# Optimization experiments

Hardware: AMD Instinct MI355X
Metric: run time of the kernel (lower is better)

The kernel has to match this reference:

```python
import jax, jax.numpy as jnp
import numpy as np

N = 100000   # nodes
E = 800000   # edges
D = 64       # feature dim (input=hidden=output)
EPS = 1e-5   # BatchNorm eps


def setup_inputs() -> dict:
    key = jax.random.key(0)
    ks = jax.random.split(key, 24)
    s = 1.0 / np.sqrt(D)
    inp = {
        "x": jax.random.normal(ks[0], (N, D), jnp.float32),
        "edge_index": jax.random.randint(ks[1], (2, E), 0, N, jnp.int64),
        # GCNConv weights (x @ W + b after normalized aggregation)
        "W1": jax.random.normal(ks[2], (D, D), jnp.float32) * s,
        "b1": jax.random.normal(ks[3], (D,), jnp.float32) * 0.01,
        "W2": jax.random.normal(ks[4], (D, D), jnp.float32) * s,
        "b2": jax.random.normal(ks[5], (D,), jnp.float32) * 0.01,
        "W3": jax.random.normal(ks[6], (D, D), jnp.float32) * s,
        "b3": jax.random.normal(ks[7], (D,), jnp.float32) * 0.01,
        # BatchNorm1d (inference: running stats)
        "bn1_g": jax.random.uniform(ks[8], (D,), jnp.float32, 0.5, 1.5),
        "bn1_b": jax.random.normal(ks[9], (D,), jnp.float32) * 0.1,
        "bn1_m": jax.random.normal(ks[10], (D,), jnp.float32) * 0.1,
        "bn1_v": jax.random.uniform(ks[11], (D,), jnp.float32, 0.5, 1.5),
        "bn2_g": jax.random.uniform(ks[12], (D,), jnp.float32, 0.5, 1.5),
        "bn2_b": jax.random.normal(ks[13], (D,), jnp.float32) * 0.1,
        "bn2_m": jax.random.normal(ks[14], (D,), jnp.float32) * 0.1,
        "bn2_v": jax.random.uniform(ks[15], (D,), jnp.float32, 0.5, 1.5),
        # predictor MLP: Linear -> tanh -> (dropout=id) -> Linear
        "pW1": jax.random.normal(ks[16], (D, D), jnp.float32) * s,
        "pb1": jax.random.normal(ks[17], (D,), jnp.float32) * 0.01,
        "pW2": jax.random.normal(ks[18], (D, D), jnp.float32) * s,
        "pb2": jax.random.normal(ks[19], (D,), jnp.float32) * 0.01,
    }
    return inp


def _gcn_norm(edge_index):
    # add self loops, compute sym-normalized edge coefficients (PyG GCNConv)
    loop = jnp.arange(N, dtype=edge_index.dtype)
    src = jnp.concatenate([edge_index[0], loop])
    dst = jnp.concatenate([edge_index[1], loop])
    deg = jax.ops.segment_sum(jnp.ones(src.shape[0], jnp.float32), dst, num_segments=N)
    dis = jax.lax.rsqrt(deg)  # deg >= 1 due to self loops
    norm = dis[src] * dis[dst]
    return src, dst, norm


def _gcn_layer(x, src, dst, norm, W, b):
    h = x @ W                              # [N, D] small GEMM
    msg = h[src] * norm[:, None]           # [E+N, D] gather (memory bound)
    return jax.ops.segment_sum(msg, dst, num_segments=N) + b  # scatter-add


def _bn(x, g, b, m, v):
    return (x - m) * (g * jax.lax.rsqrt(v + EPS)) + b


def reference(x, edge_index, W1, b1, W2, b2, W3, b3,
              bn1_g, bn1_b, bn1_m, bn1_v, bn2_g, bn2_b, bn2_m, bn2_v,
              pW1, pb1, pW2, pb2):
    src, dst, norm = _gcn_norm(edge_index)
    h = _gcn_layer(x, src, dst, norm, W1, b1)
    h = jax.nn.relu(_bn(h, bn1_g, bn1_b, bn1_m, bn1_v))   # dropout = id (eval)
    h = _gcn_layer(h, src, dst, norm, W2, b2)
    h = jax.nn.relu(_bn(h, bn2_g, bn2_b, bn2_m, bn2_v))
    h = _gcn_layer(h, src, dst, norm, W3, b3)
    out = jnp.tanh(h @ pW1 + pb1) @ pW2 + pb2              # predictor MLP
    return out
```

## Files before the change

### kernel.cpp

```cpp
#include <hip/hip_runtime.h>
#include <hip/hip_fp16.h>

#define N_NODES 100000
#define N_EDGES 800000
#define DIM 64
#define BN_EPS 1e-5f
#define LDX 68
#define EDGE_CAP 1600000

__global__ __launch_bounds__(256) void k_cvt_count(const float* __restrict__ x,
                                                   __half* __restrict__ xh,
                                                   const int* __restrict__ dst,
                                                   int* __restrict__ deg) {
    int idx = blockIdx.x * blockDim.x + threadIdx.x;
    if (idx < 1600000) {
        float4 v = ((const float4*)x)[idx];
        unsigned int u0 = __half_as_ushort(__float2half(v.x));
        unsigned int u1 = __half_as_ushort(__float2half(v.y));
        unsigned int u2 = __half_as_ushort(__float2half(v.z));
        unsigned int u3 = __half_as_ushort(__float2half(v.w));
        ((uint2*)xh)[idx] = make_uint2(u0 | (u1 << 16), u2 | (u3 << 16));
    }
    if (idx < N_EDGES) atomicAdd(&deg[dst[idx]], 1);
}

__global__ __launch_bounds__(256) void k_scan_fuse(const int* __restrict__ deg,
                                                   int* __restrict__ row_off,
                                                   int* __restrict__ cursor,
                                                   float* __restrict__ dinv,
                                                   int* __restrict__ gcount,
                                                   const float* __restrict__ W3,
                                                   const float* __restrict__ b3,
                                                   const float* __restrict__ pW1,
                                                   const float* __restrict__ pb1,
                                                   float* __restrict__ W3p,
                                                   float* __restrict__ b3p) {
    int tid = threadIdx.x;
    if (blockIdx.x == 98) {
        int c = tid & 63;
        int kbase = (tid >> 6) * 16;
        for (int k = kbase; k < kbase + 16; ++k) {
            float acc = 0.f;
#pragma unroll 8
            for (int j = 0; j < 64; ++j)
                acc = fmaf(W3[k * 64 + j], pW1[j * 64 + c], acc);
            W3p[k * 64 + c] = acc;
        }
        if (tid < 64) {
            float acc = pb1[c];
#pragma unroll 8
            for (int j = 0; j < 64; ++j)
                acc = fmaf(b3[j], pW1[j * 64 + c], acc);
            b3p[c] = acc;
        }
        return;
    }
    __shared__ int sdata[256];
    __shared__ int sbase;
    int base = blockIdx.x * 1024 + tid * 4;
    int4 d = make_int4(0, 0, 0, 0);
    int4 v = make_int4(0, 0, 0, 0);
    if (base < N_NODES) {
        d = *(const int4*)(deg + base);
        v.x = (d.x + 7) & ~7;
        v.y = (d.y + 7) & ~7;
        v.z = (d.z + 7) & ~7;
        v.w = (d.w + 7) & ~7;
    }
    int tsum = v.x + v.y + v.z + v.w;
    sdata[tid] = tsum;
    __syncthreads();
    for (int off = 1; off < 256; off <<= 1) {
        int t = (tid >= off) ? sdata[tid - off] : 0;
        __syncthreads();
        sdata[tid] += t;
        __syncthreads();
    }
    if (tid == 255) sbase = atomicAdd(gcount, sdata[255]);
    __syncthreads();
    if (base >= N_NODES) return;
    int excl = sdata[tid] - tsum + sbase;
    int4 o;
    o.x = excl;
    o.y = o.x + v.x;
    o.z = o.y + v.y;
    o.w = o.z + v.z;
    *(int4*)(row_off + base) = o;
    *(int4*)(cursor + base) = o;
    float4 di;
    di.x = rsqrtf((float)(d.x + 1));
    di.y = rsqrtf((float)(d.y + 1));
    di.z = rsqrtf((float)(d.z + 1));
    di.w = rsqrtf((float)(d.w + 1));
    *(float4*)(dinv + base) = di;
}

__global__ __launch_bounds__(256) void k_build(const int* __restrict__ ei,
                                               const float* __restrict__ dinv,
                                               int* __restrict__ cursor,
                                               int2* __restrict__ edges) {
    int part = blockIdx.x & 7;
    int e = (blockIdx.x >> 3) * 256 + threadIdx.x;
    if (e >= N_EDGES) return;
    int d = ei[N_EDGES + e];
    if (d / 12500 != part) return;
    int s = ei[e];
    int pos = atomicAdd(&cursor[d], 1);
    edges[pos] = make_int2(s, __float_as_int(dinv[s] * dinv[d]));
}

__global__ __launch_bounds__(256) void k_aggregate(const __half* __restrict__ xin,
                                                   const int* __restrict__ row_off,
                                                   const int* __restrict__ deg,
                                                   const int2* __restrict__ edges,
                                                   const float* __restrict__ dinv,
                                                   __half* __restrict__ out) {
    int lane = threadIdx.x & 63;
    int node = blockIdx.x * 4 + (threadIdx.x >> 6);
    float di = dinv[node];
    float acc = __half2float(xin[(size_t)node * DIM + lane]) * (di * di);
    int beg = __builtin_amdgcn_readfirstlane(row_off[node]);
    int lenp = (__builtin_amdgcn_readfirstlane(deg[node]) + 7) & ~7;
    int end = beg + lenp;
    for (int k = beg; k < end; k += 8) {
        int2 e0 = edges[k + 0];
        int2 e1 = edges[k + 1];
        int2 e2 = edges[k + 2];
        int2 e3 = edges[k + 3];
        int2 e4 = edges[k + 4];
        int2 e5 = edges[k + 5];
        int2 e6 = edges[k + 6];
        int2 e7 = edges[k + 7];
        float v0 = __half2float(xin[(size_t)e0.x * DIM + lane]);
        float v1 = __half2float(xin[(size_t)e1.x * DIM + lane]);
        float v2 = __half2float(xin[(size_t)e2.x * DIM + lane]);
        float v3 = __half2float(xin[(size_t)e3.x * DIM + lane]);
        float v4 = __half2float(xin[(size_t)e4.x * DIM + lane]);
        float v5 = __half2float(xin[(size_t)e5.x * DIM + lane]);
        float v6 = __half2float(xin[(size_t)e6.x * DIM + lane]);
        float v7 = __half2float(xin[(size_t)e7.x * DIM + lane]);
        acc = fmaf(__int_as_float(e0.y), v0, acc);
        acc = fmaf(__int_as_float(e1.y), v1, acc);
        acc = fmaf(__int_as_float(e2.y), v2, acc);
        acc = fmaf(__int_as_float(e3.y), v3, acc);
        acc = fmaf(__int_as_float(e4.y), v4, acc);
        acc = fmaf(__int_as_float(e5.y), v5, acc);
        acc = fmaf(__int_as_float(e6.y), v6, acc);
        acc = fmaf(__int_as_float(e7.y), v7, acc);
    }
    out[(size_t)node * DIM + lane] = __float2half(acc);
}

#define GEMM_STEP(SX, SW)                                                      \
    {                                                                          \
        float4 a0 = *(const float4*)&SX[(r0 + 0) * LDX + k4 * 4];              \
        float4 a1 = *(const float4*)&SX[(r0 + 1) * LDX + k4 * 4];              \
        float4 a2 = *(const float4*)&SX[(r0 + 2) * LDX + k4 * 4];              \
        float4 a3 = *(const float4*)&SX[(r0 + 3) * LDX + k4 * 4];              \
        float4 b0 = *(const float4*)&SW[(k4 * 4 + 0) * 64 + c0];               \
        float4 b1 = *(const float4*)&SW[(k4 * 4 + 1) * 64 + c0];               \
        float4 b2 = *(const float4*)&SW[(k4 * 4 + 2) * 64 + c0];               \
        float4 b3 = *(const float4*)&SW[(k4 * 4 + 3) * 64 + c0];               \
        const float* ap[4] = {&a0.x, &a1.x, &a2.x, &a3.x};                     \
        _Pragma("unroll") for (int i = 0; i < 4; ++i) {                        \
            float x0 = ap[i][0], x1 = ap[i][1], x2 = ap[i][2], x3 = ap[i][3];  \
            acc[i][0] = fmaf(x0, b0.x, acc[i][0]);                             \
            acc[i][1] = fmaf(x0, b0.y, acc[i][1]);                             \
            acc[i][2] = fmaf(x0, b0.z, acc[i][2]);                             \
            acc[i][3] = fmaf(x0, b0.w, acc[i][3]);                             \
            acc[i][0] = fmaf(x1, b1.x, acc[i][0]);                             \
            acc[i][1] = fmaf(x1, b1.y, acc[i][1]);                             \
            acc[i][2] = fmaf(x1, b1.z, acc[i][2]);                             \
            acc[i][3] = fmaf(x1, b1.w, acc[i][3]);                             \
            acc[i][0] = fmaf(x2, b2.x, acc[i][0]);                             \
            acc[i][1] = fmaf(x2, b2.y, acc[i][1]);                             \
            acc[i][2] = fmaf(x2, b2.z, acc[i][2]);                             \
            acc[i][3] = fmaf(x2, b2.w, acc[i][3]);                             \
            acc[i][0] = fmaf(x3, b3.x, acc[i][0]);                             \
            acc[i][1] = fmaf(x3, b3.y, acc[i][1]);                             \
            acc[i][2] = fmaf(x3, b3.z, acc[i][2]);                             \
            acc[i][3] = fmaf(x3, b3.w, acc[i][3]);                             \
        }                                                                      \
    }

#define STAGE_H2F(SRCPTR, SXPTR)                                               \
    {                                                                          \
        int r = tid >> 2;                                                      \
        int q = tid & 3;                                                       \
        int row = row0 + r;                                                    \
        float4* dst = (float4*)(SXPTR + r * LDX);                              \
        if (row < N_NODES) {                                                   \
            const uint2* src = (const uint2*)(SRCPTR + (size_t)row * DIM);     \
            _Pragma("unroll") for (int m = 0; m < 4; ++m) {                    \
                uint2 u = src[q + m * 4];                                      \
                float4 f;                                                      \
                f.x = __half2float(__ushort_as_half((unsigned short)(u.x & 0xffff)));       \
                f.y = __half2float(__ushort_as_half((unsigned short)(u.x >> 16)));          \
                f.z = __half2float(__ushort_as_half((unsigned short)(u.y & 0xffff)));       \
                f.w = __half2float(__ushort_as_half((unsigned short)(u.y >> 16)));          \
                dst[q + m * 4] = f;                                            \
            }                                                                  \
        } else {                                                               \
            float4 z = make_float4(0.f, 0.f, 0.f, 0.f);                        \
            _Pragma("unroll") for (int m = 0; m < 4; ++m) dst[q + m * 4] = z;  \
        }                                                                      \
    }

__global__ __launch_bounds__(256) void k_gemm_bn_h(const __half* __restrict__ xin,
                                                   const float* __restrict__ W,
                                                   const float* __restrict__ bias,
                                                   const float* __restrict__ bng,
                                                   const float* __restrict__ bnb,
                                                   const float* __restrict__ bnm,
                                                   const float* __restrict__ bnv,
                                                   __half* __restrict__ out) {
    __shared__ float sW[4096];
    __shared__ float sX[64 * LDX];
    int tid = threadIdx.x;
    int row0 = blockIdx.x * 64;

    for (int i = tid; i < 1024; i += 256)
        ((float4*)sW)[i] = ((const float4*)W)[i];
    STAGE_H2F(xin, sX)
    __syncthreads();

    int cq = tid & 15, rq = tid >> 4;
    int c0 = cq * 4, r0 = rq * 4;
    float acc[4][4];
#pragma unroll
    for (int i = 0; i < 4; ++i)
#pragma unroll
        for (int j = 0; j < 4; ++j) acc[i][j] = 0.f;

#pragma unroll 4
    for (int k4 = 0; k4 < 16; ++k4) GEMM_STEP(sX, sW)

    float4 bv = *(const float4*)&bias[c0];
    float4 g = *(const float4*)&bng[c0];
    float4 bb = *(const float4*)&bnb[c0];
    float4 m = *(const float4*)&bnm[c0];
    float4 vv = *(const float4*)&bnv[c0];
    float A0 = g.x * rsqrtf(vv.x + BN_EPS);
    float A1 = g.y * rsqrtf(vv.y + BN_EPS);
    float A2 = g.z * rsqrtf(vv.z + BN_EPS);
    float A3 = g.w * rsqrtf(vv.w + BN_EPS);
    float B0 = (bv.x - m.x) * A0 + bb.x;
    float B1 = (bv.y - m.y) * A1 + bb.y;
    float B2 = (bv.z - m.z) * A2 + bb.z;
    float B3 = (bv.w - m.w) * A3 + bb.w;
#pragma unroll
    for (int i = 0; i < 4; ++i) {
        int row = row0 + r0 + i;
        if (row >= N_NODES) break;
        unsigned int u0 = __half_as_ushort(__float2half(fmaxf(0.f, fmaf(acc[i][0], A0, B0))));
        unsigned int u1 = __half_as_ushort(__float2half(fmaxf(0.f, fmaf(acc[i][1], A1, B1))));
        unsigned int u2 = __half_as_ushort(__float2half(fmaxf(0.f, fmaf(acc[i][2], A2, B2))));
        unsigned int u3 = __half_as_ushort(__float2half(fmaxf(0.f, fmaf(acc[i][3], A3, B3))));
        *(uint2*)(out + (size_t)row * DIM + c0) = make_uint2(u0 | (u1 << 16), u2 | (u3 << 16));
    }
}

__global__ __launch_bounds__(256) void k_tail(const __half* __restrict__ xin,
                                              const float* __restrict__ W3p,
                                              const float* __restrict__ b3p,
                                              const float* __restrict__ pW2,
                                              const float* __restrict__ pb2,
                                              float* __restrict__ out) {
    __shared__ float sW1[4096];
    __shared__ float sW2[4096];
    __shared__ float sX[64 * LDX];
    int tid = threadIdx.x;
    int row0 = blockIdx.x * 64;

    for (int i = tid; i < 1024; i += 256) {
        ((float4*)sW1)[i] = ((const float4*)W3p)[i];
        ((float4*)sW2)[i] = ((const float4*)pW2)[i];
    }
    STAGE_H2F(xin, sX)
    __syncthreads();

    int cq = tid & 15, rq = tid >> 4;
    int c0 = cq * 4, r0 = rq * 4;
    float acc[4][4];

#pragma unroll
    for (int i = 0; i < 4; ++i)
#pragma unroll
        for (int j = 0; j < 4; ++j) acc[i][j] = 0.f;
#pragma unroll 4
    for (int k4 = 0; k4 < 16; ++k4) GEMM_STEP(sX, sW1)
    __syncthreads();

    {
        float4 bv = *(const float4*)&b3p[c0];
#pragma unroll
        for (int i = 0; i < 4; ++i) {
            float4 h;
            h.x = tanhf(acc[i][0] + bv.x);
            h.y = tanhf(acc[i][1] + bv.y);
            h.z = tanhf(acc[i][2] + bv.z);
            h.w = tanhf(acc[i][3] + bv.w);
            *(float4*)&sX[(r0 + i) * LDX + c0] = h;
        }
    }
    __syncthreads();

#pragma unroll
    for (int i = 0; i < 4; ++i)
#pragma unroll
        for (int j = 0; j < 4; ++j) acc[i][j] = 0.f;
#pragma unroll 4
    for (int k4 = 0; k4 < 16; ++k4) GEMM_STEP(sX, sW2)

    float4 bv = *(const float4*)&pb2[c0];
#pragma unroll
    for (int i = 0; i < 4; ++i) {
        int row = row0 + r0 + i;
        if (row >= N_NODES) break;
        float4 o;
        o.x = acc[i][0] + bv.x;
        o.y = acc[i][1] + bv.y;
        o.z = acc[i][2] + bv.z;
        o.w = acc[i][3] + bv.w;
        *(float4*)(out + (size_t)row * DIM + c0) = o;
    }
}

extern "C" void kernel_launch(void* const* d_in, const int* in_sizes, int n_in,
                              void* d_out, int out_size, void* d_ws, size_t ws_size,
                              hipStream_t stream) {
    const float* x     = (const float*)d_in[0];
    const int*   ei    = (const int*)d_in[1];
    const float* W1    = (const float*)d_in[2];
    const float* b1    = (const float*)d_in[3];
    const float* W2    = (const float*)d_in[4];
    const float* b2    = (const float*)d_in[5];
    const float* W3    = (const float*)d_in[6];
    const float* b3    = (const float*)d_in[7];
    const float* bn1_g = (const float*)d_in[8];
    const float* bn1_b = (const float*)d_in[9];
    const float* bn1_m = (const float*)d_in[10];
    const float* bn1_v = (const float*)d_in[11];
    const float* bn2_g = (const float*)d_in[12];
    const float* bn2_b = (const float*)d_in[13];
    const float* bn2_m = (const float*)d_in[14];
    const float* bn2_v = (const float*)d_in[15];
    const float* pW1   = (const float*)d_in[16];
    const float* pb1   = (const float*)d_in[17];
    const float* pW2   = (const float*)d_in[18];
    const float* pb2   = (const float*)d_in[19];
    float* out = (float*)d_out;

    char* ws = (char*)d_ws;
    int*    deg     = (int*)ws;                      ws += 100352 * 4;
    int*    gcount  = (int*)ws;                      ws += 4 * 4;
    int*    row_off = (int*)ws;                      ws += 100352 * 4;
    int*    cursor  = (int*)ws;                      ws += 100352 * 4;
    int2*   edges   = (int2*)ws;                     ws += (size_t)EDGE_CAP * 8;
    float*  dinv    = (float*)ws;                    ws += 100352 * 4;
    float*  W3p     = (float*)ws;                    ws += 4096 * 4;
    float*  b3p     = (float*)ws;                    ws += 64 * 4;
    __half* xh      = (__half*)ws;                   ws += (size_t)N_NODES * DIM * 2;
    __half* hbuf    = (__half*)ws;                   ws += (size_t)N_NODES * DIM * 2;
    __half* abuf    = (__half*)ws;                   ws += (size_t)N_NODES * DIM * 2;

    const int blk = 256;
    int gCvt   = 6250;
    int gBuild = 3125 * 8;
    int gAgg   = N_NODES / 4;
    int gTile  = (N_NODES + 63) / 64;

    size_t zbytes = (size_t)(100352 * 3 + 4) * 4 + (size_t)EDGE_CAP * 8;
    hipMemsetAsync(deg, 0, zbytes, stream);
    k_cvt_count<<<gCvt, blk, 0, stream>>>(x, xh, ei + N_EDGES, deg);
    k_scan_fuse<<<99, blk, 0, stream>>>(deg, row_off, cursor, dinv, gcount,
                                        W3, b3, pW1, pb1, W3p, b3p);
    k_build<<<gBuild, blk, 0, stream>>>(ei, dinv, cursor, edges);

    k_aggregate<<<gAgg, blk, 0, stream>>>(xh, row_off, deg, edges, dinv, abuf);
    k_gemm_bn_h<<<gTile, blk, 0, stream>>>(abuf, W1, b1, bn1_g, bn1_b, bn1_m, bn1_v, hbuf);

    k_aggregate<<<gAgg, blk, 0, stream>>>(hbuf, row_off, deg, edges, dinv, abuf);
    k_gemm_bn_h<<<gTile, blk, 0, stream>>>(abuf, W2, b2, bn2_g, bn2_b, bn2_m, bn2_v, hbuf);

    k_aggregate<<<gAgg, blk, 0, stream>>>(hbuf, row_off, deg, edges, dinv, abuf);
    k_tail<<<gTile, blk, 0, stream>>>(abuf, W3p, b3p, pW2, pb2, out);
}
```

Measured before the change: 367.0 us.

## Fuse neighbor aggregation into GEMM/BN and tail kernels, drop padded edge memset

Aggregation now runs inside the GEMM+BN and tail kernels. Each wavefront aggregates 16 nodes into the shared-memory tile, which removes the intermediate half-precision buffer write and read and three kernel launches. The edge loop gains an exact remainder loop instead of padding to multiples of 8, so the large memset that zeroed the edge array is shrunk to just the degree counters. The trade-off is that aggregation now runs with only 4 waves per 64-node tile, processed serially. That may reduce memory-level parallelism and occupancy for the latency-bound gather.

```diff
diff --git a/kernel.cpp b/kernel.cpp
--- a/kernel.cpp
+++ b/kernel.cpp
@@ -109,20 +109,19 @@
     edges[pos] = make_int2(s, __float_as_int(dinv[s] * dinv[d]));
 }
 
-__global__ __launch_bounds__(256) void k_aggregate(const __half* __restrict__ xin,
-                                                   const int* __restrict__ row_off,
-                                                   const int* __restrict__ deg,
-                                                   const int2* __restrict__ edges,
-                                                   const float* __restrict__ dinv,
-                                                   __half* __restrict__ out) {
-    int lane = threadIdx.x & 63;
-    int node = blockIdx.x * 4 + (threadIdx.x >> 6);
+__device__ __forceinline__ float agg_one(const __half* __restrict__ xin,
+                                         const int* __restrict__ row_off,
+                                         const int* __restrict__ deg,
+                                         const int2* __restrict__ edges,
+                                         const float* __restrict__ dinv,
+                                         int node, int lane) {
     float di = dinv[node];
     float acc = __half2float(xin[(size_t)node * DIM + lane]) * (di * di);
     int beg = __builtin_amdgcn_readfirstlane(row_off[node]);
-    int lenp = (__builtin_amdgcn_readfirstlane(deg[node]) + 7) & ~7;
-    int end = beg + lenp;
-    for (int k = beg; k < end; k += 8) {
+    int len = __builtin_amdgcn_readfirstlane(deg[node]);
+    int k = beg;
+    int kend8 = beg + (len & ~7);
+    for (; k < kend8; k += 8) {
         int2 e0 = edges[k + 0];
         int2 e1 = edges[k + 1];
         int2 e2 = edges[k + 2];
@@ -148,8 +147,28 @@
         acc = fmaf(__int_as_float(e6.y), v6, acc);
         acc = fmaf(__int_as_float(e7.y), v7, acc);
     }
-    out[(size_t)node * DIM + lane] = __float2half(acc);
-}
+    int rem = len & 7;
+    for (int j = 0; j < rem; ++j) {
+        int2 e = edges[k + j];
+        acc = fmaf(__int_as_float(e.y),
+                   __half2float(xin[(size_t)e.x * DIM + lane]), acc);
+    }
+    return acc;
+}
+
+#define AGG_TILE(SXPTR)                                                        \
+    {                                                                          \
+        int lane = tid & 63;                                                   \
+        int wv = tid >> 6;                                                     \
+        for (int n = 0; n < 16; ++n) {                                         \
+            int r = wv * 16 + n;                                               \
+            int node = row0 + r;                                               \
+            float a = 0.f;                                                     \
+            if (node < N_NODES)                                                \
+                a = agg_one(xin, row_off, deg, edges, dinv, node, lane);       \
+            SXPTR[r * LDX + lane] = a;                                         \
+        }                                                                      \
+    }
 
 #define GEMM_STEP(SX, SW)                                                      \
     {                                                                          \
@@ -183,37 +202,18 @@
         }                                                                      \
     }
 
-#define STAGE_H2F(SRCPTR, SXPTR)                                               \
-    {                                                                          \
-        int r = tid >> 2;                                                      \
-        int q = tid & 3;                                                       \
-        int row = row0 + r;                                                    \
-        float4* dst = (float4*)(SXPTR + r * LDX);                              \
-        if (row < N_NODES) {                                                   \
-            const uint2* src = (const uint2*)(SRCPTR + (size_t)row * DIM);     \
-            _Pragma("unroll") for (int m = 0; m < 4; ++m) {                    \
-                uint2 u = src[q + m * 4];                                      \
-                float4 f;                                                      \
-                f.x = __half2float(__ushort_as_half((unsigned short)(u.x & 0xffff)));       \
-                f.y = __half2float(__ushort_as_half((unsigned short)(u.x >> 16)));          \
-                f.z = __half2float(__ushort_as_half((unsigned short)(u.y & 0xffff)));       \
-                f.w = __half2float(__ushort_as_half((unsigned short)(u.y >> 16)));          \
-                dst[q + m * 4] = f;                                            \
-            }                                                                  \
-        } else {                                                               \
-            float4 z = make_float4(0.f, 0.f, 0.f, 0.f);                        \
-            _Pragma("unroll") for (int m = 0; m < 4; ++m) dst[q + m * 4] = z;  \
-        }                                                                      \
-    }
-
-__global__ __launch_bounds__(256) void k_gemm_bn_h(const __half* __restrict__ xin,
-                                                   const float* __restrict__ W,
-                                                   const float* __restrict__ bias,
-                                                   const float* __restrict__ bng,
-                                                   const float* __restrict__ bnb,
-                                                   const float* __restrict__ bnm,
-                                                   const float* __restrict__ bnv,
-                                                   __half* __restrict__ out) {
+__global__ __launch_bounds__(256) void k_agg_gemm_bn(const __half* __restrict__ xin,
+                                                     const int* __restrict__ row_off,
+                                                     const int* __restrict__ deg,
+                                                     const int2* __restrict__ edges,
+                                                     const float* __restrict__ dinv,
+                                                     const float* __restrict__ W,
+                                                     const float* __restrict__ bias,
+                                                     const float* __restrict__ bng,
+                                                     const float* __restrict__ bnb,
+                                                     const float* __restrict__ bnm,
+                                                     const float* __restrict__ bnv,
+                                                     __half* __restrict__ out) {
     __shared__ float sW[4096];
     __shared__ float sX[64 * LDX];
     int tid = threadIdx.x;
@@ -221,7 +221,7 @@
 
     for (int i = tid; i < 1024; i += 256)
         ((float4*)sW)[i] = ((const float4*)W)[i];
-    STAGE_H2F(xin, sX)
+    AGG_TILE(sX)
     __syncthreads();
 
     int cq = tid & 15, rq = tid >> 4;
@@ -260,12 +260,16 @@
     }
 }
 
-__global__ __launch_bounds__(256) void k_tail(const __half* __restrict__ xin,
-                                              const float* __restrict__ W3p,
-                                              const float* __restrict__ b3p,
-                                              const float* __restrict__ pW2,
-                                              const float* __restrict__ pb2,
-                                              float* __restrict__ out) {
+__global__ __launch_bounds__(256) void k_agg_tail(const __half* __restrict__ xin,
+                                                  const int* __restrict__ row_off,
+                                                  const int* __restrict__ deg,
+                                                  const int2* __restrict__ edges,
+                                                  const float* __restrict__ dinv,
+                                                  const float* __restrict__ W3p,
+                                                  const float* __restrict__ b3p,
+                                                  const float* __restrict__ pW2,
+                                                  const float* __restrict__ pb2,
+                                                  float* __restrict__ out) {
     __shared__ float sW1[4096];
     __shared__ float sW2[4096];
     __shared__ float sX[64 * LDX];
@@ -276,7 +280,7 @@
         ((float4*)sW1)[i] = ((const float4*)W3p)[i];
         ((float4*)sW2)[i] = ((const float4*)pW2)[i];
     }
-    STAGE_H2F(xin, sX)
+    AGG_TILE(sX)
     __syncthreads();
 
     int cq = tid & 15, rq = tid >> 4;
@@ -362,27 +366,22 @@
     float*  b3p     = (float*)ws;                    ws += 64 * 4;
     __half* xh      = (__half*)ws;                   ws += (size_t)N_NODES * DIM * 2;
     __half* hbuf    = (__half*)ws;                   ws += (size_t)N_NODES * DIM * 2;
-    __half* abuf    = (__half*)ws;                   ws += (size_t)N_NODES * DIM * 2;
 
     const int blk = 256;
     int gCvt   = 6250;
     int gBuild = 3125 * 8;
-    int gAgg   = N_NODES / 4;
     int gTile  = (N_NODES + 63) / 64;
 
-    size_t zbytes = (size_t)(100352 * 3 + 4) * 4 + (size_t)EDGE_CAP * 8;
-    hipMemsetAsync(deg, 0, zbytes, stream);
+    hipMemsetAsync(deg, 0, (size_t)(100352 + 4) * 4, stream);
     k_cvt_count<<<gCvt, blk, 0, stream>>>(x, xh, ei + N_EDGES, deg);
     k_scan_fuse<<<99, blk, 0, stream>>>(deg, row_off, cursor, dinv, gcount,
                                         W3, b3, pW1, pb1, W3p, b3p);
     k_build<<<gBuild, blk, 0, stream>>>(ei, dinv, cursor, edges);
 
-    k_aggregate<<<gAgg, blk, 0, stream>>>(xh, row_off, deg, edges, dinv, abuf);
-    k_gemm_bn_h<<<gTile, blk, 0, stream>>>(abuf, W1, b1, bn1_g, bn1_b, bn1_m, bn1_v, hbuf);
-
-    k_aggregate<<<gAgg, blk, 0, stream>>>(hbuf, row_off, deg, edges, dinv, abuf);
-    k_gemm_bn_h<<<gTile, blk, 0, stream>>>(abuf, W2, b2, bn2_g, bn2_b, bn2_m, bn2_v, hbuf);
-
-    k_aggregate<<<gAgg, blk, 0, stream>>>(hbuf, row_off, deg, edges, dinv, abuf);
-    k_tail<<<gTile, blk, 0, stream>>>(abuf, W3p, b3p, pW2, pb2, out);
-}
+    k_agg_gemm_bn<<<gTile, blk, 0, stream>>>(xh, row_off, deg, edges, dinv,
+                                             W1, b1, bn1_g, bn1_b, bn1_m, bn1_v, hbuf);
+    k_agg_gemm_bn<<<gTile, blk, 0, stream>>>(hbuf, row_off, deg, edges, dinv,
+                                             W2, b2, bn2_g, bn2_b, bn2_m, bn2_v, xh);
+    k_agg_tail<<<gTile, blk, 0, stream>>>(xh, row_off, deg, edges, dinv,
+                                          W3p, b3p, pW2, pb2, out);
+}
```

New measurement: 510.5 us. +39.1%, slower.

## Aggregate with 16 lanes per node using 8-byte half loads; shrink memset

Applied to the files above, without the earlier changes.

The aggregation kernel now assigns 16 lanes per node instead of a full 64-lane wave. Each lane gathers four halves with one 8-byte load, so each wave processes four nodes at once. Neighbor lists are no longer padded to multiples of 8. Instead the loop runs to the wave-wide max degree, clamps the index and zeroes the weight for lanes past their own degree. The memset drops from the whole edge array plus padding to just the degree counters. Divergent degrees within a wave cause some wasted gathers, and the code relies on the clamp and a source bounds check because padded edge slots are no longer zeroed.

```diff
diff --git a/kernel.cpp b/kernel.cpp
--- a/kernel.cpp
+++ b/kernel.cpp
@@ -115,40 +115,46 @@
                                                    const int2* __restrict__ edges,
                                                    const float* __restrict__ dinv,
                                                    __half* __restrict__ out) {
-    int lane = threadIdx.x & 63;
-    int node = blockIdx.x * 4 + (threadIdx.x >> 6);
+    int lane16 = threadIdx.x & 15;
+    int node = blockIdx.x * 16 + (threadIdx.x >> 4);
     float di = dinv[node];
-    float acc = __half2float(xin[(size_t)node * DIM + lane]) * (di * di);
-    int beg = __builtin_amdgcn_readfirstlane(row_off[node]);
-    int lenp = (__builtin_amdgcn_readfirstlane(deg[node]) + 7) & ~7;
-    int end = beg + lenp;
-    for (int k = beg; k < end; k += 8) {
-        int2 e0 = edges[k + 0];
-        int2 e1 = edges[k + 1];
-        int2 e2 = edges[k + 2];
-        int2 e3 = edges[k + 3];
-        int2 e4 = edges[k + 4];
-        int2 e5 = edges[k + 5];
-        int2 e6 = edges[k + 6];
-        int2 e7 = edges[k + 7];
-        float v0 = __half2float(xin[(size_t)e0.x * DIM + lane]);
-        float v1 = __half2float(xin[(size_t)e1.x * DIM + lane]);
-        float v2 = __half2float(xin[(size_t)e2.x * DIM + lane]);
-        float v3 = __half2float(xin[(size_t)e3.x * DIM + lane]);
-        float v4 = __half2float(xin[(size_t)e4.x * DIM + lane]);
-        float v5 = __half2float(xin[(size_t)e5.x * DIM + lane]);
-        float v6 = __half2float(xin[(size_t)e6.x * DIM + lane]);
-        float v7 = __half2float(xin[(size_t)e7.x * DIM + lane]);
-        acc = fmaf(__int_as_float(e0.y), v0, acc);
-        acc = fmaf(__int_as_float(e1.y), v1, acc);
-        acc = fmaf(__int_as_float(e2.y), v2, acc);
-        acc = fmaf(__int_as_float(e3.y), v3, acc);
-        acc = fmaf(__int_as_float(e4.y), v4, acc);
-        acc = fmaf(__int_as_float(e5.y), v5, acc);
-        acc = fmaf(__int_as_float(e6.y), v6, acc);
-        acc = fmaf(__int_as_float(e7.y), v7, acc);
-    }
-    out[(size_t)node * DIM + lane] = __float2half(acc);
+    int beg = row_off[node];
+    int len = deg[node];
+
+    uint2 us = ((const uint2*)(xin + (size_t)node * DIM))[lane16];
+    float w0 = di * di;
+    float4 acc;
+    acc.x = __half2float(__ushort_as_half((unsigned short)(us.x & 0xffff))) * w0;
+    acc.y = __half2float(__ushort_as_half((unsigned short)(us.x >> 16))) * w0;
+    acc.z = __half2float(__ushort_as_half((unsigned short)(us.y & 0xffff))) * w0;
+    acc.w = __half2float(__ushort_as_half((unsigned short)(us.y >> 16))) * w0;
+
+    int lenmax = len;
+    lenmax = max(lenmax, __shfl_xor(lenmax, 16, 64));
+    lenmax = max(lenmax, __shfl_xor(lenmax, 32, 64));
+
+    int lclamp = (len > 0) ? (len - 1) : 0;
+    for (int i = 0; i < lenmax; i += 8) {
+#pragma unroll
+        for (int u = 0; u < 8; ++u) {
+            int j = i + u;
+            int jc = j < lclamp ? j : lclamp;
+            int2 e = edges[beg + jc];
+            int s = ((unsigned)e.x < N_NODES) ? e.x : 0;
+            float w = (j < len) ? __int_as_float(e.y) : 0.f;
+            uint2 u2 = ((const uint2*)(xin + (size_t)s * DIM))[lane16];
+            acc.x = fmaf(w, __half2float(__ushort_as_half((unsigned short)(u2.x & 0xffff))), acc.x);
+            acc.y = fmaf(w, __half2float(__ushort_as_half((unsigned short)(u2.x >> 16))), acc.y);
+            acc.z = fmaf(w, __half2float(__ushort_as_half((unsigned short)(u2.y & 0xffff))), acc.z);
+            acc.w = fmaf(w, __half2float(__ushort_as_half((unsigned short)(u2.y >> 16))), acc.w);
+        }
+    }
+
+    unsigned int p0 = __half_as_ushort(__float2half(acc.x)) |
+                      (__half_as_ushort(__float2half(acc.y)) << 16);
+    unsigned int p1 = __half_as_ushort(__float2half(acc.z)) |
+                      (__half_as_ushort(__float2half(acc.w)) << 16);
+    ((uint2*)(out + (size_t)node * DIM))[lane16] = make_uint2(p0, p1);
 }
 
 #define GEMM_STEP(SX, SW)                                                      \
@@ -367,11 +373,10 @@
     const int blk = 256;
     int gCvt   = 6250;
     int gBuild = 3125 * 8;
-    int gAgg   = N_NODES / 4;
+    int gAgg   = N_NODES / 16;
     int gTile  = (N_NODES + 63) / 64;
 
-    size_t zbytes = (size_t)(100352 * 3 + 4) * 4 + (size_t)EDGE_CAP * 8;
-    hipMemsetAsync(deg, 0, zbytes, stream);
+    hipMemsetAsync(deg, 0, (size_t)(100352 + 4) * 4, stream);
     k_cvt_count<<<gCvt, blk, 0, stream>>>(x, xh, ei + N_EDGES, deg);
     k_scan_fuse<<<99, blk, 0, stream>>>(deg, row_off, cursor, dinv, gcount,
                                         W3, b3, pW1, pb1, W3p, b3p);
```

Result: slower. 389.5 us (+6.1%).
